# Kernel tuning notes

Measured on AMD Instinct MI355X. Metric: run time of the kernel, lower is better.

The kernel has to match this reference:

```python
import jax, jax.numpy as jnp
import numpy as np

B, D, N, K, T = 8192, 256, 2048, 512, 8
M_MARGIN = 1.0
LAMBDA_ORTHO = 1e-3
EPS = 1e-10


def _l2(a, b):
    # squared L2 distance along last axis
    return jnp.sum((a - b) ** 2, axis=-1)


def setup_inputs() -> dict:
    key = jax.random.key(0)
    k1, k2, k3, k4, k5 = jax.random.split(key, 5)
    return {
        "v": jax.random.normal(k1, (B, D), dtype=jnp.float32),
        "vhat": jax.random.normal(k2, (B, D), dtype=jnp.float32),
        "g": jax.random.uniform(k3, (B, K), dtype=jnp.float32),
        "F": jax.random.normal(k4, (K, D), dtype=jnp.float32),
        "negatives": jax.random.normal(k5, (N, D), dtype=jnp.float32),
        "mask": jnp.ones((B,), dtype=bool),
    }


def reference(v, vhat, g, F, negatives, mask):
    maskf = mask.astype(v.dtype)
    msum = maskf.sum()

    # ---- contrastive loss (vectorized over the N-negatives loop) ----
    true_dist = _l2(vhat, v)                                   # [B]
    neg_dist = _l2(vhat[:, None, :], negatives[None, :, :])    # [B, N]
    per = jnp.maximum(1.0 + true_dist[:, None] - neg_dist, 0.0)
    ju_per = per.mean(axis=1) * maskf                          # [B]
    Ju = jnp.where(msum == 0, 0.0, ju_per.sum() / msum)

    # ---- focal triplet loss (topk smallest g, gather F rows) ----
    _, idx = jax.lax.top_k(-g, T)                              # [B, T] indices of t smallest
    g_tz = jnp.take_along_axis(g, idx, axis=1)                 # [B, T]
    F_t = F[idx]                                               # [B, T, D]
    g_t = g_tz / (g_tz.sum(axis=1, keepdims=True) + EPS)
    m_t = M_MARGIN * (1.0 - g_t) ** 2                          # [B, T]
    d_neg = _l2(vhat[:, None, :], F_t)                         # [B, T]
    cur = jnp.maximum(m_t + true_dist[:, None] - d_neg, 0.0)
    jt_per = cur.sum(axis=1) * maskf
    Jt = jnp.where(msum == 0, 0.0, jt_per.sum() / msum)

    # ---- orthogonality regularizer: ||F F^T - I||_F, then squared ----
    gram = F @ F.T - jnp.eye(K, dtype=F.dtype)
    ortho = jnp.sqrt(jnp.sum(gram ** 2))

    Jz = Ju + Jt + LAMBDA_ORTHO * ortho ** 2
    return Jz
```

## Files before the change

### kernel.cpp

```cpp
#include <hip/hip_runtime.h>

#define B_N 8192
#define D_N 256
#define N_N 2048
#define K_N 512
#define T_N 8

using short8  = __attribute__((ext_vector_type(8))) short;
using floatx4 = __attribute__((ext_vector_type(4))) float;


__device__ __forceinline__ float wave_reduce_sum(float x) {
  #pragma unroll
  for (int off = 32; off > 0; off >>= 1) x += __shfl_xor(x, off, 64);
  return x;
}

__device__ __forceinline__ unsigned int f2bf(float x) {
  unsigned u = __float_as_uint(x);
  return (u + 0x7fffu + ((u >> 16) & 1u)) >> 16;
}

__device__ __forceinline__ unsigned int pack2bf(float x, float y) {
  return f2bf(x) | (f2bf(y) << 16);
}

__device__ __forceinline__ void gload16(const unsigned short* g, unsigned short* l) {
  __builtin_amdgcn_global_load_lds(
      (const __attribute__((address_space(1))) unsigned int*)g,
      (__attribute__((address_space(3))) unsigned int*)l, 16, 0, 0);
}

#define CSWAP(a, b)                                              \
  {                                                              \
    bool sw_ = sv[a] > sv[b];                                    \
    float tv_ = sw_ ? sv[a] : sv[b];                             \
    sv[a] = sw_ ? sv[b] : sv[a];                                 \
    sv[b] = tv_;                                                 \
    int ti_ = sw_ ? si[a] : si[b];                               \
    si[a] = sw_ ? si[b] : si[a];                                 \
    si[b] = ti_;                                                 \
  }

__global__ __launch_bounds__(256) void prep_kernel(
    const float* __restrict__ v, const float* __restrict__ vhat,
    const float* __restrict__ neg, const float* __restrict__ F,
    const float* __restrict__ g, const int* __restrict__ mask,
    unsigned short* __restrict__ vhat_bf, unsigned short* __restrict__ neg_bf,
    unsigned short* __restrict__ F_bf,
    float* __restrict__ cb, float* __restrict__ nn2, float* __restrict__ fn2,
    float* __restrict__ jt_part, float* __restrict__ msum_part,
    float* __restrict__ acc, int* __restrict__ cnt) {
  int lane = threadIdx.x & 63;
  int wave = threadIdx.x >> 6;
  int row = (blockIdx.x << 2) + wave;
  __shared__ float mred[4];
  __shared__ float jred[4];
  if (blockIdx.x == 0 && threadIdx.x == 0) {
    acc[0] = 0.0f; acc[1] = 0.0f; *cnt = 0;
  }
  if (blockIdx.x < 32) {
    float m = (mask[blockIdx.x * 256 + threadIdx.x] != 0) ? 1.0f : 0.0f;
    m = wave_reduce_sum(m);
    if (lane == 0) mred[wave] = m;
    __syncthreads();
    if (threadIdx.x == 0)
      msum_part[blockIdx.x] = mred[0] + mred[1] + mred[2] + mred[3];
  }
  if (row < B_N) {
    const float4 a = *(const float4*)(vhat + (size_t)row * D_N + lane * 4);
    const float4 b = *(const float4*)(v + (size_t)row * D_N + lane * 4);
    float dx = a.x - b.x, dy = a.y - b.y, dz = a.z - b.z, dw = a.w - b.w;
    float t = dx * dx + dy * dy + dz * dz + dw * dw;
    float n = a.x * a.x + a.y * a.y + a.z * a.z + a.w * a.w;
    uint2 p;
    p.x = pack2bf(a.x, a.y);
    p.y = pack2bf(a.z, a.w);
    *(uint2*)(vhat_bf + (size_t)row * D_N + lane * 4) = p;
    t = wave_reduce_sum(t);
    n = wave_reduce_sum(n);
    if (lane == 0) cb[row] = 1.0f + t - n;
    const float* grow = g + (size_t)row * K_N;
    float sv[8];
    int si[8];
    {
      float4 g0 = *(const float4*)(grow + lane * 8);
      float4 g1 = *(const float4*)(grow + lane * 8 + 4);
      sv[0] = g0.x; sv[1] = g0.y; sv[2] = g0.z; sv[3] = g0.w;
      sv[4] = g1.x; sv[5] = g1.y; sv[6] = g1.z; sv[7] = g1.w;
      #pragma unroll
      for (int j = 0; j < 8; ++j) si[j] = lane * 8 + j;
    }
    CSWAP(0,1) CSWAP(2,3) CSWAP(4,5) CSWAP(6,7)
    CSWAP(0,2) CSWAP(1,3) CSWAP(4,6) CSWAP(5,7)
    CSWAP(1,2) CSWAP(5,6)
    CSWAP(0,4) CSWAP(1,5) CSWAP(2,6) CSWAP(3,7)
    CSWAP(2,4) CSWAP(3,5)
    CSWAP(1,2) CSWAP(3,4) CSWAP(5,6)
    #pragma unroll
    for (int rr = 0; rr < 6; ++rr) {
      const int msk = 1 << rr;
      float pv[8];
      int pi[8];
      #pragma unroll
      for (int j = 0; j < 8; ++j) {
        pv[j] = __shfl_xor(sv[j], msk, 64);
        pi[j] = __shfl_xor(si[j], msk, 64);
      }
      float cv[8];
      int ci[8];
      #pragma unroll
      for (int j = 0; j < 8; ++j) {
        bool mine = sv[j] <= pv[7 - j];
        cv[j] = mine ? sv[j] : pv[7 - j];
        ci[j] = mine ? si[j] : pi[7 - j];
      }
      #pragma unroll
      for (int j = 0; j < 8; ++j) { sv[j] = cv[j]; si[j] = ci[j]; }
      CSWAP(0,4) CSWAP(1,5) CSWAP(2,6) CSWAP(3,7)
      CSWAP(0,2) CSWAP(1,3) CSWAP(4,6) CSWAP(5,7)
      CSWAP(0,1) CSWAP(2,3) CSWAP(4,5) CSWAP(6,7)
    }
    float4 fr8[8];
    #pragma unroll
    for (int t8 = 0; t8 < T_N; ++t8) {
      int idx = __builtin_amdgcn_readfirstlane(si[t8]);
      fr8[t8] = *(const float4*)(F + (size_t)idx * D_N + lane * 4);
    }
    float gsum = 1e-10f;
    #pragma unroll
    for (int t8 = 0; t8 < T_N; ++t8) gsum += sv[t8];
    float base = t - n;
    float jts = 0.0f;
    #pragma unroll
    for (int t8 = 0; t8 < T_N; ++t8) {
      float4 f = fr8[t8];
      float s = 2.0f * (a.x * f.x + a.y * f.y + a.z * f.z + a.w * f.w)
              - (f.x * f.x + f.y * f.y + f.z * f.z + f.w * f.w);
      s = wave_reduce_sum(s);
      float gt = sv[t8] / gsum;
      float mt = 1.0f - gt;
      mt *= mt;
      jts += fmaxf(mt + base + s, 0.0f);
    }
    float mf = (mask[row] != 0) ? 1.0f : 0.0f;
    if (lane == 0) jred[wave] = jts * mf;
    __syncthreads();
    if (threadIdx.x == 0)
      jt_part[blockIdx.x] = jred[0] + jred[1] + jred[2] + jred[3];
  } else if (row < B_N + N_N) {
    int r = row - B_N;
    const float4 a = *(const float4*)(neg + (size_t)r * D_N + lane * 4);
    float n = a.x * a.x + a.y * a.y + a.z * a.z + a.w * a.w;
    uint2 p;
    p.x = pack2bf(a.x, a.y);
    p.y = pack2bf(a.z, a.w);
    *(uint2*)(neg_bf + (size_t)r * D_N + lane * 4) = p;
    n = wave_reduce_sum(n);
    if (lane == 0) nn2[r] = n;
  } else {
    int r = row - (B_N + N_N);
    const float4 a = *(const float4*)(F + (size_t)r * D_N + lane * 4);
    float n = a.x * a.x + a.y * a.y + a.z * a.z + a.w * a.w;
    uint2 p;
    p.x = pack2bf(a.x, a.y);
    p.y = pack2bf(a.z, a.w);
    *(uint2*)(F_bf + (size_t)r * D_N + lane * 4) = p;
    n = wave_reduce_sum(n);
    if (lane == 0) fn2[r] = n;
  }
}

__global__ __launch_bounds__(256) void main_kernel(
    const unsigned short* __restrict__ vhat_bf, const unsigned short* __restrict__ neg_bf,
    const unsigned short* __restrict__ F_bf,
    const float* __restrict__ cb, const float* __restrict__ nn2,
    const float* __restrict__ fn2, const int* __restrict__ mask,
    const float* __restrict__ jt_part, const float* __restrict__ msum_part,
    float* __restrict__ acc, int* __restrict__ cnt, float* __restrict__ out) {
  __shared__ __align__(16) unsigned char smem[16384];
  __shared__ int lastFlag;
  const int bx = blockIdx.x;
  const int tid = threadIdx.x;
  const int lane = tid & 63;
  const int wave = tid >> 6;

  unsigned short* AsU = (unsigned short*)smem;
  unsigned short* BsU = AsU + 4096;
  int r0, c0;
  const unsigned short *Abase, *Bbase;
  int seg;
  float wgt = 1.0f;
  if (bx < 10) {
    seg = 1;
    int o = bx;
    int ti = (o < 4) ? 0 : (o < 7) ? 1 : (o < 9) ? 2 : 3;
    int tj = (o < 4) ? o : (o < 7) ? o - 3 : (o < 9) ? o - 5 : 3;
    r0 = ti * 128;
    c0 = tj * 128;
    wgt = (ti == tj) ? 1.0f : 2.0f;
    Abase = F_bf;
    Bbase = F_bf;
  } else {
    seg = 0;
    int o = bx - 10;
    r0 = (o >> 4) * 128;
    c0 = (o & 15) * 128;
    Abase = vhat_bf;
    Bbase = neg_bf;
  }
  const int wx = wave & 1, wy = wave >> 1;

  const int c_slot = lane & 3;
  const int rA0 = wave * 32 + (lane >> 2);
  const int rA1 = rA0 + 16;
  const int cg0 = c_slot ^ ((rA0 >> 1) & 3);
  const int cg1 = c_slot ^ ((rA1 >> 1) & 3);
  const unsigned short* gA0 = Abase + (size_t)(r0 + rA0) * D_N + cg0 * 8;
  const unsigned short* gA1 = Abase + (size_t)(r0 + rA1) * D_N + cg1 * 8;
  const unsigned short* gB0 = Bbase + (size_t)(c0 + rA0) * D_N + cg0 * 8;
  const unsigned short* gB1 = Bbase + (size_t)(c0 + rA1) * D_N + cg1 * 8;
  unsigned short* lA0 = AsU + wave * 1024 + lane * 8;
  unsigned short* lA1 = lA0 + 512;
  unsigned short* lB0 = BsU + wave * 1024 + lane * 8;
  unsigned short* lB1 = lB0 + 512;

  const int fr = lane & 15;
  const int fc = lane >> 4;
  int aoff[4], boff[4];
  #pragma unroll
  for (int i = 0; i < 4; ++i) {
    int ra = wy * 64 + i * 16 + fr;
    aoff[i] = ra * 32 + (fc ^ ((ra >> 1) & 3)) * 8;
    int rb = wx * 64 + i * 16 + fr;
    boff[i] = rb * 32 + (fc ^ ((rb >> 1) & 3)) * 8;
  }

  floatx4 acc4[4][4];
  #pragma unroll
  for (int i = 0; i < 4; ++i)
    #pragma unroll
    for (int j = 0; j < 4; ++j)
      acc4[i][j] = floatx4{0.0f, 0.0f, 0.0f, 0.0f};

  for (int k0 = 0; k0 < D_N; k0 += 32) {
    __syncthreads();
    gload16(gA0 + k0, lA0);
    gload16(gA1 + k0, lA1);
    gload16(gB0 + k0, lB0);
    gload16(gB1 + k0, lB1);
    __syncthreads();
    short8 af[4], bf[4];
    #pragma unroll
    for (int i = 0; i < 4; ++i) af[i] = *(const short8*)(AsU + aoff[i]);
    #pragma unroll
    for (int j = 0; j < 4; ++j) bf[j] = *(const short8*)(BsU + boff[j]);
    #pragma unroll
    for (int i = 0; i < 4; ++i)
      #pragma unroll
      for (int j = 0; j < 4; ++j)
        acc4[i][j] = __builtin_amdgcn_mfma_f32_16x16x32_bf16(af[i], bf[j], acc4[i][j], 0, 0, 0);
  }

  float lsum = 0.0f;
  if (seg == 0) {
    float nns[4];
    #pragma unroll
    for (int j = 0; j < 4; ++j)
      nns[j] = nn2[c0 + wx * 64 + j * 16 + (lane & 15)];
    #pragma unroll
    for (int i = 0; i < 4; ++i) {
      #pragma unroll
      for (int r = 0; r < 4; ++r) {
        int b = r0 + wy * 64 + i * 16 + (lane >> 4) * 4 + r;
        float cbb = cb[b];
        float mf = (mask[b] != 0) ? 1.0f : 0.0f;
        float rs = 0.0f;
        #pragma unroll
        for (int j = 0; j < 4; ++j) {
          float val = cbb + 2.0f * acc4[i][j][r] - nns[j];
          rs += fmaxf(val, 0.0f);
        }
        lsum += mf * rs;
      }
    }
  } else {
    #pragma unroll
    for (int i = 0; i < 4; ++i) {
      #pragma unroll
      for (int r = 0; r < 4; ++r) {
        int gi = r0 + wy * 64 + i * 16 + (lane >> 4) * 4 + r;
        #pragma unroll
        for (int j = 0; j < 4; ++j) {
          int gj = c0 + wx * 64 + j * 16 + (lane & 15);
          float s = (gi == gj) ? (fn2[gi] - 1.0f) : acc4[i][j][r];
          lsum += s * s;
        }
      }
    }
    lsum *= wgt;
  }

  lsum = wave_reduce_sum(lsum);
  float* red = (float*)smem;
  __syncthreads();
  if (lane == 0) red[wave] = lsum;
  __syncthreads();
  if (tid == 0) {
    float partial = red[0] + red[1] + red[2] + red[3];
    atomicAdd(&acc[seg == 0 ? 0 : 1], partial);
    __threadfence();
    lastFlag = (atomicAdd(cnt, 1) == (int)gridDim.x - 1) ? 1 : 0;
  }
  __syncthreads();
  if (lastFlag) {
    __threadfence();
    float sjt = 0.0f, sm = 0.0f;
    for (int i = tid; i < 2048; i += 256) sjt += jt_part[i];
    if (tid < 32) sm = msum_part[tid];
    sjt = wave_reduce_sum(sjt);
    sm = wave_reduce_sum(sm);
    __syncthreads();
    if (lane == 0) { red[wave] = sjt; red[4 + wave] = sm; }
    __syncthreads();
    if (tid == 0) {
      float jt = red[0] + red[1] + red[2] + red[3];
      float ms = red[4] + red[5] + red[6] + red[7];
      float ju = atomicAdd(&acc[0], 0.0f);
      float oo = atomicAdd(&acc[1], 0.0f);
      float Ju = (ms == 0.0f) ? 0.0f : ju / ((float)N_N * ms);
      float Jt = (ms == 0.0f) ? 0.0f : jt / ms;
      out[0] = Ju + Jt + 1.0e-3f * oo;
    }
  }
}

extern "C" void kernel_launch(void* const* d_in, const int* in_sizes, int n_in,
                              void* d_out, int out_size, void* d_ws, size_t ws_size,
                              hipStream_t stream) {
  (void)in_sizes; (void)n_in; (void)out_size; (void)ws_size;
  const float* v    = (const float*)d_in[0];
  const float* vhat = (const float*)d_in[1];
  const float* g    = (const float*)d_in[2];
  const float* F    = (const float*)d_in[3];
  const float* neg  = (const float*)d_in[4];
  const int*   mask = (const int*)d_in[5];

  float* ws = (float*)d_ws;
  float* cb        = ws;
  float* nn2       = ws + 8192;
  float* fn2       = ws + 10240;
  float* jt_part   = ws + 10752;
  float* msum_part = ws + 12800;
  float* acc       = ws + 12832;
  int*   cnt       = (int*)(ws + 12834);
  unsigned short* vhat_bf = (unsigned short*)(ws + 12848);
  unsigned short* neg_bf  = vhat_bf + (size_t)B_N * D_N;
  unsigned short* F_bf    = neg_bf + (size_t)N_N * D_N;

  prep_kernel<<<(B_N + N_N + K_N) / 4, 256, 0, stream>>>(
      v, vhat, neg, F, g, mask, vhat_bf, neg_bf, F_bf, cb, nn2, fn2,
      jt_part, msum_part, acc, cnt);
  main_kernel<<<10 + 1024, 256, 0, stream>>>(
      vhat_bf, neg_bf, F_bf, cb, nn2, fn2, mask, jt_part, msum_part,
      acc, cnt, (float*)d_out);
}
```

Baseline: 138.1 us.

## Replace atomic last-block reduction with per-block partials and finalize kernel; remap tile order

Each main-kernel block now writes its partial sum to its own slot instead of doing global atomicAdds and a last-block counter. A separate single-block finalize kernel reduces all partials and writes the output. The block-to-tile mapping for the contrastive GEMM is also permuted so that consecutive blocks spread across row tiles, which changes L2 reuse of the shared operands. The cost removed is the atomic contention and fences at each block's end. In exchange it adds an extra kernel launch and loses the overlap of the final reduction with the tail of the main kernel.

```diff
diff --git a/kernel.cpp b/kernel.cpp
--- a/kernel.cpp
+++ b/kernel.cpp
@@ -49,16 +49,12 @@
     unsigned short* __restrict__ vhat_bf, unsigned short* __restrict__ neg_bf,
     unsigned short* __restrict__ F_bf,
     float* __restrict__ cb, float* __restrict__ nn2, float* __restrict__ fn2,
-    float* __restrict__ jt_part, float* __restrict__ msum_part,
-    float* __restrict__ acc, int* __restrict__ cnt) {
+    float* __restrict__ jt_part, float* __restrict__ msum_part) {
   int lane = threadIdx.x & 63;
   int wave = threadIdx.x >> 6;
   int row = (blockIdx.x << 2) + wave;
   __shared__ float mred[4];
   __shared__ float jred[4];
-  if (blockIdx.x == 0 && threadIdx.x == 0) {
-    acc[0] = 0.0f; acc[1] = 0.0f; *cnt = 0;
-  }
   if (blockIdx.x < 32) {
     float m = (mask[blockIdx.x * 256 + threadIdx.x] != 0) ? 1.0f : 0.0f;
     m = wave_reduce_sum(m);
@@ -176,10 +172,8 @@
     const unsigned short* __restrict__ F_bf,
     const float* __restrict__ cb, const float* __restrict__ nn2,
     const float* __restrict__ fn2, const int* __restrict__ mask,
-    const float* __restrict__ jt_part, const float* __restrict__ msum_part,
-    float* __restrict__ acc, int* __restrict__ cnt, float* __restrict__ out) {
+    float* __restrict__ ju_part, float* __restrict__ or_part) {
   __shared__ __align__(16) unsigned char smem[16384];
-  __shared__ int lastFlag;
   const int bx = blockIdx.x;
   const int tid = threadIdx.x;
   const int lane = tid & 63;
@@ -187,7 +181,7 @@
 
   unsigned short* AsU = (unsigned short*)smem;
   unsigned short* BsU = AsU + 4096;
-  int r0, c0;
+  int r0, c0, lo = 0;
   const unsigned short *Abase, *Bbase;
   int seg;
   float wgt = 1.0f;
@@ -204,8 +198,9 @@
   } else {
     seg = 0;
     int o = bx - 10;
-    r0 = (o >> 4) * 128;
-    c0 = (o & 15) * 128;
+    lo = (o & 7) * 128 + (o >> 3);
+    r0 = (lo >> 4) * 128;
+    c0 = (lo & 15) * 128;
     Abase = vhat_bf;
     Bbase = neg_bf;
   }
@@ -308,30 +303,39 @@
   __syncthreads();
   if (tid == 0) {
     float partial = red[0] + red[1] + red[2] + red[3];
-    atomicAdd(&acc[seg == 0 ? 0 : 1], partial);
-    __threadfence();
-    lastFlag = (atomicAdd(cnt, 1) == (int)gridDim.x - 1) ? 1 : 0;
+    if (seg == 0) ju_part[lo] = partial;
+    else or_part[bx] = partial;
+  }
+}
+
+__global__ __launch_bounds__(256) void finalize_kernel(
+    const float* __restrict__ jt_part, const float* __restrict__ ju_part,
+    const float* __restrict__ or_part, const float* __restrict__ msum_part,
+    float* __restrict__ out) {
+  int tid = threadIdx.x;
+  float sjt = 0.0f, sju = 0.0f, sor = 0.0f, sm = 0.0f;
+  for (int i = tid; i < 2048; i += 256) sjt += jt_part[i];
+  for (int i = tid; i < 1024; i += 256) sju += ju_part[i];
+  if (tid < 10) sor = or_part[tid];
+  if (tid < 32) sm = msum_part[tid];
+  sjt = wave_reduce_sum(sjt);
+  sju = wave_reduce_sum(sju);
+  sor = wave_reduce_sum(sor);
+  sm  = wave_reduce_sum(sm);
+  __shared__ float red[4][4];
+  int lane = tid & 63, w = tid >> 6;
+  if (lane == 0) {
+    red[w][0] = sjt; red[w][1] = sju; red[w][2] = sor; red[w][3] = sm;
   }
   __syncthreads();
-  if (lastFlag) {
-    __threadfence();
-    float sjt = 0.0f, sm = 0.0f;
-    for (int i = tid; i < 2048; i += 256) sjt += jt_part[i];
-    if (tid < 32) sm = msum_part[tid];
-    sjt = wave_reduce_sum(sjt);
-    sm = wave_reduce_sum(sm);
-    __syncthreads();
-    if (lane == 0) { red[wave] = sjt; red[4 + wave] = sm; }
-    __syncthreads();
-    if (tid == 0) {
-      float jt = red[0] + red[1] + red[2] + red[3];
-      float ms = red[4] + red[5] + red[6] + red[7];
-      float ju = atomicAdd(&acc[0], 0.0f);
-      float oo = atomicAdd(&acc[1], 0.0f);
-      float Ju = (ms == 0.0f) ? 0.0f : ju / ((float)N_N * ms);
-      float Jt = (ms == 0.0f) ? 0.0f : jt / ms;
-      out[0] = Ju + Jt + 1.0e-3f * oo;
-    }
+  if (tid == 0) {
+    float jt = red[0][0] + red[1][0] + red[2][0] + red[3][0];
+    float ju = red[0][1] + red[1][1] + red[2][1] + red[3][1];
+    float oo = red[0][2] + red[1][2] + red[2][2] + red[3][2];
+    float ms = red[0][3] + red[1][3] + red[2][3] + red[3][3];
+    float Ju = (ms == 0.0f) ? 0.0f : ju / ((float)N_N * ms);
+    float Jt = (ms == 0.0f) ? 0.0f : jt / ms;
+    out[0] = Ju + Jt + 1.0e-3f * oo;
   }
 }
 
@@ -352,16 +356,17 @@
   float* fn2       = ws + 10240;
   float* jt_part   = ws + 10752;
   float* msum_part = ws + 12800;
-  float* acc       = ws + 12832;
-  int*   cnt       = (int*)(ws + 12834);
-  unsigned short* vhat_bf = (unsigned short*)(ws + 12848);
+  float* ju_part   = ws + 12832;
+  float* or_part   = ws + 13856;
+  unsigned short* vhat_bf = (unsigned short*)(ws + 13872);
   unsigned short* neg_bf  = vhat_bf + (size_t)B_N * D_N;
   unsigned short* F_bf    = neg_bf + (size_t)N_N * D_N;
 
   prep_kernel<<<(B_N + N_N + K_N) / 4, 256, 0, stream>>>(
       v, vhat, neg, F, g, mask, vhat_bf, neg_bf, F_bf, cb, nn2, fn2,
-      jt_part, msum_part, acc, cnt);
+      jt_part, msum_part);
   main_kernel<<<10 + 1024, 256, 0, stream>>>(
-      vhat_bf, neg_bf, F_bf, cb, nn2, fn2, mask, jt_part, msum_part,
-      acc, cnt, (float*)d_out);
-}
+      vhat_bf, neg_bf, F_bf, cb, nn2, fn2, mask, ju_part, or_part);
+  finalize_kernel<<<1, 256, 0, stream>>>(jt_part, ju_part, or_part, msum_part,
+                                         (float*)d_out);
+}
```

Result: faster. 114.4 us (-17.2%).
